# Kernel optimization log

Measured on AMD Instinct MI355X. Metric: run time of the kernel, lower is better.

The kernel has to match this reference:

```python
import jax, jax.numpy as jnp
import numpy as np
from jax import lax

N_QUBITS = 8
N_LAYERS = 7


def _conv(x, w, b, stride, pad):
    y = lax.conv_general_dilated(x, w, (stride, stride), [(pad, pad), (pad, pad)],
                                 dimension_numbers=('NCHW', 'OIHW', 'NCHW'))
    return y + b[None, :, None, None]


def _apply_1q(psi, M, q):
    # psi: (B, 2,2,...,2); apply 2x2 real matrix M on qubit q (axis q+1)
    a = q + 1
    pm = jnp.moveaxis(psi, a, 1)
    out = jnp.einsum('ij,bj...->bi...', M, pm)
    return jnp.moveaxis(out, 1, a)


def _apply_cnot(psi, c, t):
    ac, at = c + 1, t + 1
    pm = jnp.moveaxis(psi, (ac, at), (1, 2))
    top = pm[:, 0]
    bot = jnp.flip(pm[:, 1], axis=1)  # flip target when control=1
    pm = jnp.stack([top, bot], axis=1)
    return jnp.moveaxis(pm, (1, 2), (ac, at))


def _quantum(features, qw):
    psi = features / jnp.linalg.norm(features, axis=1, keepdims=True)
    B = psi.shape[0]
    psi = psi.reshape((B,) + (2,) * N_QUBITS)
    for l in range(N_LAYERS):
        for q in range(N_QUBITS):
            th = qw[l, q] / 2.0
            c, s = jnp.cos(th), jnp.sin(th)
            M = jnp.stack([jnp.stack([c, -s]), jnp.stack([s, c])])
            psi = _apply_1q(psi, M, q)
        for q in range(N_QUBITS - 1):
            psi = _apply_cnot(psi, q, q + 1)
    p = psi.reshape(B, 2, -1) ** 2
    return jnp.sum(p[:, 0], axis=1) - jnp.sum(p[:, 1], axis=1)  # <PauliZ(0)>


def setup_inputs() -> dict:
    key = jax.random.key(0)
    ks = jax.random.split(key, 20)
    def g(k, shape, fan_in):
        return jax.random.normal(k, shape, jnp.float32) * (1.0 / np.sqrt(fan_in))
    inp = {
        'x':  jax.random.normal(ks[0], (4096, 1, 64, 64), jnp.float32),
        'w1': g(ks[1], (4, 1, 5, 5), 25), 'b1': jnp.zeros((4,), jnp.float32),
        'w2': g(ks[2], (8, 4, 3, 3), 36), 'b2': jnp.zeros((8,), jnp.float32),
        'w3': g(ks[3], (16, 8, 3, 3), 72), 'b3': jnp.zeros((16,), jnp.float32),
        'wf': g(ks[4], (256, 64), 64), 'bf': jnp.zeros((256,), jnp.float32),
        'qw': jax.random.uniform(ks[5], (7, 8), jnp.float32, 0.0, 2 * np.pi),
        'wc1': g(ks[6], (200, 1), 1),   'bc1': jnp.zeros((200,), jnp.float32),
        'wc2': g(ks[7], (150, 200), 200), 'bc2': jnp.zeros((150,), jnp.float32),
        'wc3': g(ks[8], (100, 150), 150), 'bc3': jnp.zeros((100,), jnp.float32),
        'wc4': g(ks[9], (50, 100), 100),  'bc4': jnp.zeros((50,), jnp.float32),
        'wc5': g(ks[10], (1, 50), 50),    'bc5': jnp.zeros((1,), jnp.float32),
    }
    return inp


def reference(x, w1, b1, w2, b2, w3, b3, wf, bf, qw,
              wc1, bc1, wc2, bc2, wc3, bc3, wc4, bc4, wc5, bc5):
    # CNN feature extractor (dropout = identity at inference)
    h = jax.nn.relu(_conv(x, w1, b1, 2, 2))   # (B,4,32,32)
    h = jax.nn.relu(_conv(h, w2, b2, 2, 1))   # (B,8,16,16)
    h = jax.nn.relu(_conv(h, w3, b3, 1, 1))   # (B,16,16,16)
    B = h.shape[0]
    # AdaptiveAvgPool2d(2): 16x16 -> 2x2 via 8x8 non-overlapping means
    h = h.reshape(B, 16, 2, 8, 2, 8).mean(axis=(3, 5))  # (B,16,2,2)
    h = h.reshape(B, 64)
    feats = jax.nn.relu(h @ wf.T + bf)        # (B,256)
    # F.normalize(p=2, dim=1)
    feats = feats / jnp.maximum(jnp.linalg.norm(feats, axis=1, keepdims=True), 1e-12)
    # Batched 8-qubit statevector simulation (replaces per-sample Python loop)
    q = _quantum(feats, qw)[:, None]          # (B,1)
    # MLP classifier
    h = jax.nn.relu(q @ wc1.T + bc1)
    h = jax.nn.relu(h @ wc2.T + bc2)
    h = jax.nn.relu(h @ wc3.T + bc3)
    h = jax.nn.relu(h @ wc4.T + bc4)
    return jax.nn.sigmoid(h @ wc5.T + bc5)    # (B,1)
```

## Files before the change

kernel.cpp:

```cpp
#include <hip/hip_runtime.h>
#include <math.h>

typedef float v2f __attribute__((ext_vector_type(2)));
#define FMA2(a, b, c) __builtin_elementwise_fma((a), (b), (c))

__global__ __launch_bounds__(256, 8)
void convpool_kernel(const float* __restrict__ x,
                     const float* __restrict__ w1, const float* __restrict__ b1,
                     const float* __restrict__ w2, const float* __restrict__ b2,
                     const float* __restrict__ w3, const float* __restrict__ b3,
                     float* __restrict__ poolout)
{
    __shared__ __align__(16) float arena[4648];
    const int tid  = threadIdx.x;
    const int b    = blockIdx.x;
    const int lane = tid & 63;

    float wstage[7];
    #pragma unroll
    for (int j = 0; j < 7; j++) {
        const int s  = tid + 256 * j;
        const int oc = s / 100;
        const int r  = s - oc * 100;
        const int ic = r / 12;
        const int k  = r - ic * 12;
        wstage[j] = (s < 1600 && r < 96 && k < 9) ? w3[oc * 72 + ic * 9 + k] : 0.f;
    }
    const float bstage = (tid < 16) ? b3[tid] : 0.f;

    if (tid < 40) arena[4608 + tid] = 0.f;

    {
        const float* xb = x + (size_t)b * 4096;
        const int oh  = tid >> 3;
        const int ow  = tid & 7;
        const int ow0 = ow * 4;
        const int c0  = ow0 * 2 - 2;
        const bool cmL = (ow == 0);
        const bool cmR = (ow == 7);
        v2f aP[4][2];
        {
            const v2f b01 = {b1[0], b1[1]};
            const v2f b23 = {b1[2], b1[3]};
            #pragma unroll
            for (int p = 0; p < 4; p++) { aP[p][0] = b01; aP[p][1] = b23; }
        }
        #pragma unroll
        for (int kh = 0; kh < 5; kh++) {
            const int ih = oh * 2 - 2 + kh;
            if (ih >= 0 && ih < 64) {
                const float* row = xb + ih * 64;
                float colv[11];
                {
                    float v0 = row[cmL ? 0 : c0];
                    float v1 = row[cmL ? 0 : c0 + 1];
                    float vA = row[cmR ? 63 : c0 + 10];
                    colv[0]  = cmL ? 0.f : v0;
                    colv[1]  = cmL ? 0.f : v1;
                    colv[10] = cmR ? 0.f : vA;
                }
                {
                    const float4 m0 = *(const float4*)(row + c0 + 2);
                    const float4 m1 = *(const float4*)(row + c0 + 6);
                    colv[2] = m0.x; colv[3] = m0.y; colv[4] = m0.z; colv[5] = m0.w;
                    colv[6] = m1.x; colv[7] = m1.y; colv[8] = m1.z; colv[9] = m1.w;
                }
                #pragma unroll
                for (int kw = 0; kw < 5; kw++) {
                    const v2f w01 = {w1[kh * 5 + kw],      w1[25 + kh * 5 + kw]};
                    const v2f w23 = {w1[50 + kh * 5 + kw], w1[75 + kh * 5 + kw]};
                    #pragma unroll
                    for (int p = 0; p < 4; p++) {
                        const float c = colv[kw + 2 * p];
                        const v2f cs = {c, c};
                        aP[p][0] = FMA2(cs, w01, aP[p][0]);
                        aP[p][1] = FMA2(cs, w23, aP[p][1]);
                    }
                }
            }
        }
        const int bsw1 = (oh >> 1) & 1;
        float* obase = arena + oh * 36 + ((ow ^ bsw1) << 2);
        {
            float4 v;
            v.x = fmaxf(aP[0][0].x, 0.f); v.y = fmaxf(aP[1][0].x, 0.f);
            v.z = fmaxf(aP[2][0].x, 0.f); v.w = fmaxf(aP[3][0].x, 0.f);
            *(float4*)(obase) = v;
            v.x = fmaxf(aP[0][0].y, 0.f); v.y = fmaxf(aP[1][0].y, 0.f);
            v.z = fmaxf(aP[2][0].y, 0.f); v.w = fmaxf(aP[3][0].y, 0.f);
            *(float4*)(obase + 1152) = v;
            v.x = fmaxf(aP[0][1].x, 0.f); v.y = fmaxf(aP[1][1].x, 0.f);
            v.z = fmaxf(aP[2][1].x, 0.f); v.w = fmaxf(aP[3][1].x, 0.f);
            *(float4*)(obase + 2304) = v;
            v.x = fmaxf(aP[0][1].y, 0.f); v.y = fmaxf(aP[1][1].y, 0.f);
            v.z = fmaxf(aP[2][1].y, 0.f); v.w = fmaxf(aP[3][1].y, 0.f);
            *(float4*)(obase + 3456) = v;
        }
    }
    __syncthreads();

    v2f cacc[4];
    {
        const int oc0 = __builtin_amdgcn_readfirstlane(tid >> 6);
        const int oh  = lane >> 2;
        const int w   = lane & 3;
        {
            const v2f bb = {b2[oc0], b2[oc0 + 4]};
            #pragma unroll
            for (int p = 0; p < 4; p++) cacc[p] = bb;
        }
        #pragma unroll
        for (int ic = 0; ic < 4; ic++) {
            const float* base = arena + ic * 1152;
            const float* wA = w2 + ((oc0    ) * 4 + ic) * 9;
            const float* wB = w2 + ((oc0 + 4) * 4 + ic) * 9;
            #pragma unroll
            for (int kh = 0; kh < 3; kh++) {
                const int r2 = 2 * oh + kh - 1;
                const bool zr = (kh == 0) && (oh == 0);
                const int rc = zr ? 0 : r2;
                const int bsw = (rc >> 1) & 1;
                const float* row = zr ? (arena + 4608) : (base + rc * 36);
                const float4 qA = *(const float4*)(row + (((2 * w)     ^ bsw) << 2));
                const float4 qB = *(const float4*)(row + (((2 * w + 1) ^ bsw) << 2));
                const int sblk = (w == 0) ? bsw : ((2 * w - 1) ^ bsw);
                const float sv = row[(sblk << 2) + 3];
                float colv[9];
                colv[0] = (w == 0) ? 0.f : sv;
                colv[1] = qA.x; colv[2] = qA.y; colv[3] = qA.z; colv[4] = qA.w;
                colv[5] = qB.x; colv[6] = qB.y; colv[7] = qB.z; colv[8] = qB.w;
                #pragma unroll
                for (int kw = 0; kw < 3; kw++) {
                    const v2f wab = {wA[kh * 3 + kw], wB[kh * 3 + kw]};
                    #pragma unroll
                    for (int p = 0; p < 4; p++) {
                        const float c = colv[kw + 2 * p];
                        const v2f cs = {c, c};
                        cacc[p] = FMA2(cs, wab, cacc[p]);
                    }
                }
            }
        }
    }
    __syncthreads();

    for (int i = tid; i < 544; i += 256) {
        const int ch = i / 68, j = i - ch * 68;
        if (j < 18)      arena[ch * 360 + j] = 0.f;
        else if (j < 36) arena[ch * 360 + 17 * 20 + (j - 18)] = 0.f;
        else if (j < 52) arena[ch * 360 + (j - 35) * 20] = 0.f;
        else             arena[ch * 360 + (j - 51) * 20 + 17] = 0.f;
    }
    {
        const int oc0 = __builtin_amdgcn_readfirstlane(tid >> 6);
        const int oh  = lane >> 2, ow0 = (lane & 3) * 4;
        float* oA = arena + oc0 * 360       + (oh + 1) * 20 + ow0 + 1;
        float* oB = arena + (oc0 + 4) * 360 + (oh + 1) * 20 + ow0 + 1;
        oA[0] = fmaxf(cacc[0].x, 0.f); oA[1] = fmaxf(cacc[1].x, 0.f);
        oA[2] = fmaxf(cacc[2].x, 0.f); oA[3] = fmaxf(cacc[3].x, 0.f);
        oB[0] = fmaxf(cacc[0].y, 0.f); oB[1] = fmaxf(cacc[1].y, 0.f);
        oB[2] = fmaxf(cacc[2].y, 0.f); oB[3] = fmaxf(cacc[3].y, 0.f);
    }
    #pragma unroll
    for (int j = 0; j < 7; j++) {
        const int s = tid + 256 * j;
        if (s < 1600) arena[2880 + s] = wstage[j];
    }
    if (tid < 16) arena[4480 + tid] = bstage;
    __syncthreads();

    {
        const float* w3s = arena + 2880;
        const int oc = tid >> 4, s = tid & 15;
        const int tr = (s >> 2) * 4, tc = (s & 3) * 4;
        v2f acc2[4][2];
        const float bv = w3s[1600 + oc];
        #pragma unroll
        for (int r = 0; r < 4; r++) {
            acc2[r][0] = (v2f){bv, bv};
            acc2[r][1] = (v2f){bv, bv};
        }
        #pragma unroll
        for (int ic = 0; ic < 8; ic++) {
            const float* xc = arena + ic * 360;
            const float4 wv0 = *(const float4*)(w3s + oc * 100 + ic * 12);
            const float4 wv1 = *(const float4*)(w3s + oc * 100 + ic * 12 + 4);
            const float  wv8 = w3s[oc * 100 + ic * 12 + 8];
            const float wv[9] = {wv0.x, wv0.y, wv0.z, wv0.w, wv1.x, wv1.y, wv1.z, wv1.w, wv8};
            #pragma unroll
            for (int j = 0; j < 6; j++) {
                const float* rp = xc + (tr + j) * 20 + tc;
                const float4 qa = *(const float4*)(rp);
                const float4 qb = *(const float4*)(rp + 4);
                const v2f e0 = {qa.x, qa.y};
                const v2f o0 = {qa.y, qa.z};
                const v2f e1 = {qa.z, qa.w};
                const v2f o1 = {qa.w, qb.x};
                const v2f e2 = {qb.x, qb.y};
                #pragma unroll
                for (int r = 0; r < 4; r++) {
                    const int kh = j - r;
                    if (kh >= 0 && kh < 3) {
                        const v2f w0s = {wv[kh * 3 + 0], wv[kh * 3 + 0]};
                        const v2f w1s = {wv[kh * 3 + 1], wv[kh * 3 + 1]};
                        const v2f w2s = {wv[kh * 3 + 2], wv[kh * 3 + 2]};
                        acc2[r][0] = FMA2(e0, w0s, acc2[r][0]);
                        acc2[r][0] = FMA2(o0, w1s, acc2[r][0]);
                        acc2[r][0] = FMA2(e1, w2s, acc2[r][0]);
                        acc2[r][1] = FMA2(e1, w0s, acc2[r][1]);
                        acc2[r][1] = FMA2(o1, w1s, acc2[r][1]);
                        acc2[r][1] = FMA2(e2, w2s, acc2[r][1]);
                    }
                }
            }
        }
        float ps = 0.f;
        #pragma unroll
        for (int r = 0; r < 4; r++) {
            ps += fmaxf(acc2[r][0].x, 0.f);
            ps += fmaxf(acc2[r][0].y, 0.f);
            ps += fmaxf(acc2[r][1].x, 0.f);
            ps += fmaxf(acc2[r][1].y, 0.f);
        }
        ps += __shfl_xor(ps, 1, 64);
        ps += __shfl_xor(ps, 4, 64);
        if ((s & 5) == 0) {
            const int ii = s >> 3, jj = (s >> 1) & 1;
            poolout[b * 64 + oc * 4 + ii * 2 + jj] = ps * (1.f / 64.f);
        }
    }
}

__global__ __launch_bounds__(256)
void head_kernel(const float* __restrict__ poolin,
                 const float* __restrict__ wf, const float* __restrict__ bf,
                 const float* __restrict__ qw,
                 const float* __restrict__ wc1, const float* __restrict__ bc1,
                 const float* __restrict__ wc2, const float* __restrict__ bc2,
                 const float* __restrict__ wc3, const float* __restrict__ bc3,
                 const float* __restrict__ wc4, const float* __restrict__ bc4,
                 const float* __restrict__ wc5, const float* __restrict__ bc5,
                 float* __restrict__ out)
{
    __shared__ __align__(16) float pool_s[256];
    __shared__ __align__(16) float feats[1024];
    __shared__ __align__(16) float h1[800];
    __shared__ __align__(16) float h2[600];
    __shared__ __align__(16) float h3[400];
    __shared__ __align__(16) float h4[200];
    __shared__ float zbuf[4];
    __shared__ float csc[56], css[56];

    const int tid  = threadIdx.x;
    const int blk  = blockIdx.x;
    const int lane = tid & 63;
    const int wv   = tid >> 6;

    pool_s[tid] = poolin[(size_t)blk * 256 + tid];
    if (tid < 56) {
        float th = qw[tid] * 0.5f;
        csc[tid] = cosf(th);
        css[tid] = sinf(th);
    }
    __syncthreads();

    {
        float acc[4];
        const float bv = bf[tid];
        #pragma unroll
        for (int e = 0; e < 4; e++) acc[e] = bv;
        const float4* wr = (const float4*)(wf + tid * 64);
        #pragma unroll
        for (int kc = 0; kc < 4; kc++) {
            float4 w0 = wr[kc * 4 + 0], w1_ = wr[kc * 4 + 1], w2_ = wr[kc * 4 + 2], w3_ = wr[kc * 4 + 3];
            #pragma unroll
            for (int e = 0; e < 4; e++) {
                const float4* pp = (const float4*)(pool_s + e * 64 + kc * 16);
                float4 p0 = pp[0], p1 = pp[1], p2 = pp[2], p3 = pp[3];
                float a = acc[e];
                a = fmaf(w0.x, p0.x, a); a = fmaf(w0.y, p0.y, a); a = fmaf(w0.z, p0.z, a); a = fmaf(w0.w, p0.w, a);
                a = fmaf(w1_.x, p1.x, a); a = fmaf(w1_.y, p1.y, a); a = fmaf(w1_.z, p1.z, a); a = fmaf(w1_.w, p1.w, a);
                a = fmaf(w2_.x, p2.x, a); a = fmaf(w2_.y, p2.y, a); a = fmaf(w2_.z, p2.z, a); a = fmaf(w2_.w, p2.w, a);
                a = fmaf(w3_.x, p3.x, a); a = fmaf(w3_.y, p3.y, a); a = fmaf(w3_.z, p3.z, a); a = fmaf(w3_.w, p3.w, a);
                acc[e] = a;
            }
        }
        #pragma unroll
        for (int e = 0; e < 4; e++) feats[e * 256 + tid] = fmaxf(acc[e], 0.f);
    }
    __syncthreads();

    {
        const float* base = feats + wv * 256;
        float v0 = base[lane], v1 = base[64 + lane];
        float v2 = base[128 + lane], v3 = base[192 + lane];
        float ssq = v0 * v0 + v1 * v1 + v2 * v2 + v3 * v3;
        #pragma unroll
        for (int off = 1; off < 64; off <<= 1) ssq += __shfl_xor(ssq, off, 64);
        const float inv = 1.0f / fmaxf(sqrtf(ssq), 1e-12f);
        v0 *= inv; v1 *= inv; v2 *= inv; v3 *= inv;

        for (int l = 0; l < 7; l++) {
            {
                float c = csc[l * 8 + 0], s = css[l * 8 + 0];
                float n0 = c * v0 - s * v2, n2 = s * v0 + c * v2;
                float n1 = c * v1 - s * v3, n3 = s * v1 + c * v3;
                float c1 = csc[l * 8 + 1], s1 = css[l * 8 + 1];
                v0 = c1 * n0 - s1 * n1; v1 = s1 * n0 + c1 * n1;
                v2 = c1 * n2 - s1 * n3; v3 = s1 * n2 + c1 * n3;
            }
            #pragma unroll
            for (int q = 2; q < 8; q++) {
                const int m = 1 << (7 - q);
                const float c = csc[l * 8 + q], s = css[l * 8 + q];
                const float sgn = (lane & m) ? s : -s;
                float t0 = __shfl_xor(v0, m, 64);
                float t1 = __shfl_xor(v1, m, 64);
                float t2 = __shfl_xor(v2, m, 64);
                float t3 = __shfl_xor(v3, m, 64);
                v0 = fmaf(sgn, t0, c * v0);
                v1 = fmaf(sgn, t1, c * v1);
                v2 = fmaf(sgn, t2, c * v2);
                v3 = fmaf(sgn, t3, c * v3);
            }
            { float t = v2; v2 = v3; v3 = t; }
            v1 = __shfl_xor(v1, 32, 64);
            v3 = __shfl_xor(v3, 32, 64);
            #pragma unroll
            for (int q = 2; q < 7; q++) {
                const int mc = 1 << (7 - q), mt = 1 << (6 - q);
                float t0 = __shfl_xor(v0, mt, 64);
                float t1 = __shfl_xor(v1, mt, 64);
                float t2 = __shfl_xor(v2, mt, 64);
                float t3 = __shfl_xor(v3, mt, 64);
                if (lane & mc) { v0 = t0; v1 = t1; v2 = t2; v3 = t3; }
            }
        }
        float m0 = v0 * v0 + v1 * v1 - v2 * v2 - v3 * v3;
        #pragma unroll
        for (int off = 1; off < 64; off <<= 1) m0 += __shfl_xor(m0, off, 64);
        if (lane == 0) zbuf[wv] = m0;
    }
    __syncthreads();

    if (tid < 200) {
        const float w = wc1[tid], bv = bc1[tid];
        #pragma unroll
        for (int e = 0; e < 4; e++) h1[e * 200 + tid] = fmaxf(fmaf(zbuf[e], w, bv), 0.f);
    }
    __syncthreads();
    if (tid < 150) {
        float acc[4];
        const float bv = bc2[tid];
        #pragma unroll
        for (int e = 0; e < 4; e++) acc[e] = bv;
        const float4* wr = (const float4*)(wc2 + tid * 200);
        for (int kc = 0; kc < 25; kc++) {
            float4 wa = wr[2 * kc], wb = wr[2 * kc + 1];
            #pragma unroll
            for (int e = 0; e < 4; e++) {
                const float4* hp = (const float4*)(h1 + e * 200) + 2 * kc;
                float4 ha = hp[0], hb = hp[1];
                float a = acc[e];
                a = fmaf(wa.x, ha.x, a); a = fmaf(wa.y, ha.y, a); a = fmaf(wa.z, ha.z, a); a = fmaf(wa.w, ha.w, a);
                a = fmaf(wb.x, hb.x, a); a = fmaf(wb.y, hb.y, a); a = fmaf(wb.z, hb.z, a); a = fmaf(wb.w, hb.w, a);
                acc[e] = a;
            }
        }
        #pragma unroll
        for (int e = 0; e < 4; e++) h2[e * 150 + tid] = fmaxf(acc[e], 0.f);
    }
    __syncthreads();
    if (tid < 100) {
        float acc[4];
        const float bv = bc3[tid];
        #pragma unroll
        for (int e = 0; e < 4; e++) acc[e] = bv;
        const float2* wr = (const float2*)(wc3 + tid * 150);
        for (int k = 0; k < 75; k++) {
            float2 wa = wr[k];
            #pragma unroll
            for (int e = 0; e < 4; e++) {
                float2 hv = ((const float2*)(h2 + e * 150))[k];
                acc[e] = fmaf(wa.x, hv.x, fmaf(wa.y, hv.y, acc[e]));
            }
        }
        #pragma unroll
        for (int e = 0; e < 4; e++) h3[e * 100 + tid] = fmaxf(acc[e], 0.f);
    }
    __syncthreads();
    if (tid < 50) {
        float acc[4];
        const float bv = bc4[tid];
        #pragma unroll
        for (int e = 0; e < 4; e++) acc[e] = bv;
        const float4* wr = (const float4*)(wc4 + tid * 100);
        for (int kc = 0; kc < 25; kc++) {
            float4 wa = wr[kc];
            #pragma unroll
            for (int e = 0; e < 4; e++) {
                float4 hv = ((const float4*)(h3 + e * 100))[kc];
                float a = acc[e];
                a = fmaf(wa.x, hv.x, a); a = fmaf(wa.y, hv.y, a);
                a = fmaf(wa.z, hv.z, a); a = fmaf(wa.w, hv.w, a);
                acc[e] = a;
            }
        }
        #pragma unroll
        for (int e = 0; e < 4; e++) h4[e * 50 + tid] = fmaxf(acc[e], 0.f);
    }
    __syncthreads();
    if (tid < 4) {
        float acc = bc5[0];
        const float2* wr = (const float2*)wc5;
        #pragma unroll
        for (int k = 0; k < 25; k++) {
            float2 wa = wr[k];
            float2 hv = ((const float2*)(h4 + tid * 50))[k];
            acc = fmaf(wa.x, hv.x, fmaf(wa.y, hv.y, acc));
        }
        out[blk * 4 + tid] = 1.0f / (1.0f + expf(-acc));
    }
}

extern "C" void kernel_launch(void* const* d_in, const int* in_sizes, int n_in,
                              void* d_out, int out_size, void* d_ws, size_t ws_size,
                              hipStream_t stream) {
    const float* x   = (const float*)d_in[0];
    const float* w1  = (const float*)d_in[1];
    const float* b1  = (const float*)d_in[2];
    const float* w2  = (const float*)d_in[3];
    const float* b2  = (const float*)d_in[4];
    const float* w3  = (const float*)d_in[5];
    const float* b3  = (const float*)d_in[6];
    const float* wf  = (const float*)d_in[7];
    const float* bf  = (const float*)d_in[8];
    const float* qw  = (const float*)d_in[9];
    const float* wc1 = (const float*)d_in[10];
    const float* bc1 = (const float*)d_in[11];
    const float* wc2 = (const float*)d_in[12];
    const float* bc2 = (const float*)d_in[13];
    const float* wc3 = (const float*)d_in[14];
    const float* bc3 = (const float*)d_in[15];
    const float* wc4 = (const float*)d_in[16];
    const float* bc4 = (const float*)d_in[17];
    const float* wc5 = (const float*)d_in[18];
    const float* bc5 = (const float*)d_in[19];
    float* out = (float*)d_out;

    float* poolbuf = (float*)d_ws;

    convpool_kernel<<<4096, 256, 0, stream>>>(x, w1, b1, w2, b2, w3, b3, poolbuf);
    head_kernel<<<1024, 256, 0, stream>>>(poolbuf, wf, bf, qw,
                                          wc1, bc1, wc2, bc2, wc3, bc3,
                                          wc4, bc4, wc5, bc5, out);
}
```

Before: 212.3 us.

## Run MLP head per-wave per-sample with wave-local syncs instead of block barriers

```diff
diff --git a/kernel.cpp b/kernel.cpp
--- a/kernel.cpp
+++ b/kernel.cpp
@@ -3,6 +3,7 @@
 
 typedef float v2f __attribute__((ext_vector_type(2)));
 #define FMA2(a, b, c) __builtin_elementwise_fma((a), (b), (c))
+#define WAVE_SYNC() asm volatile("s_waitcnt lgkmcnt(0)" ::: "memory")
 
 __global__ __launch_bounds__(256, 8)
 void convpool_kernel(const float* __restrict__ x,
@@ -244,11 +245,7 @@
 {
     __shared__ __align__(16) float pool_s[256];
     __shared__ __align__(16) float feats[1024];
-    __shared__ __align__(16) float h1[800];
-    __shared__ __align__(16) float h2[600];
-    __shared__ __align__(16) float h3[400];
-    __shared__ __align__(16) float h4[200];
-    __shared__ float zbuf[4];
+    __shared__ __align__(16) float hbuf[4][512];
     __shared__ float csc[56], css[56];
 
     const int tid  = threadIdx.x;
@@ -290,6 +287,7 @@
     }
     __syncthreads();
 
+    float z;
     {
         const float* base = feats + wv * 256;
         float v0 = base[lane], v1 = base[64 + lane];
@@ -339,87 +337,81 @@
         float m0 = v0 * v0 + v1 * v1 - v2 * v2 - v3 * v3;
         #pragma unroll
         for (int off = 1; off < 64; off <<= 1) m0 += __shfl_xor(m0, off, 64);
-        if (lane == 0) zbuf[wv] = m0;
-    }
-    __syncthreads();
-
-    if (tid < 200) {
-        const float w = wc1[tid], bv = bc1[tid];
-        #pragma unroll
-        for (int e = 0; e < 4; e++) h1[e * 200 + tid] = fmaxf(fmaf(zbuf[e], w, bv), 0.f);
-    }
-    __syncthreads();
-    if (tid < 150) {
-        float acc[4];
-        const float bv = bc2[tid];
-        #pragma unroll
-        for (int e = 0; e < 4; e++) acc[e] = bv;
-        const float4* wr = (const float4*)(wc2 + tid * 200);
-        for (int kc = 0; kc < 25; kc++) {
-            float4 wa = wr[2 * kc], wb = wr[2 * kc + 1];
-            #pragma unroll
-            for (int e = 0; e < 4; e++) {
-                const float4* hp = (const float4*)(h1 + e * 200) + 2 * kc;
-                float4 ha = hp[0], hb = hp[1];
-                float a = acc[e];
+        z = m0;
+    }
+
+    float* H = hbuf[wv];
+
+    #pragma unroll
+    for (int t = 0; t < 4; t++) {
+        const int j = lane + 64 * t;
+        if (j < 200) H[j] = fmaxf(fmaf(z, wc1[j], bc1[j]), 0.f);
+    }
+    WAVE_SYNC();
+
+    #pragma unroll
+    for (int t = 0; t < 3; t++) {
+        const int j = lane + 64 * t;
+        if (j < 150) {
+            float a = bc2[j];
+            const float4* wr = (const float4*)(wc2 + j * 200);
+            const float4* hp = (const float4*)(H);
+            #pragma unroll 5
+            for (int kc = 0; kc < 25; kc++) {
+                const float4 wa = wr[2 * kc], wb = wr[2 * kc + 1];
+                const float4 ha = hp[2 * kc], hb = hp[2 * kc + 1];
                 a = fmaf(wa.x, ha.x, a); a = fmaf(wa.y, ha.y, a); a = fmaf(wa.z, ha.z, a); a = fmaf(wa.w, ha.w, a);
                 a = fmaf(wb.x, hb.x, a); a = fmaf(wb.y, hb.y, a); a = fmaf(wb.z, hb.z, a); a = fmaf(wb.w, hb.w, a);
-                acc[e] = a;
-            }
-        }
-        #pragma unroll
-        for (int e = 0; e < 4; e++) h2[e * 150 + tid] = fmaxf(acc[e], 0.f);
-    }
-    __syncthreads();
-    if (tid < 100) {
-        float acc[4];
-        const float bv = bc3[tid];
-        #pragma unroll
-        for (int e = 0; e < 4; e++) acc[e] = bv;
-        const float2* wr = (const float2*)(wc3 + tid * 150);
-        for (int k = 0; k < 75; k++) {
-            float2 wa = wr[k];
-            #pragma unroll
-            for (int e = 0; e < 4; e++) {
-                float2 hv = ((const float2*)(h2 + e * 150))[k];
-                acc[e] = fmaf(wa.x, hv.x, fmaf(wa.y, hv.y, acc[e]));
-            }
-        }
-        #pragma unroll
-        for (int e = 0; e < 4; e++) h3[e * 100 + tid] = fmaxf(acc[e], 0.f);
-    }
-    __syncthreads();
-    if (tid < 50) {
-        float acc[4];
-        const float bv = bc4[tid];
-        #pragma unroll
-        for (int e = 0; e < 4; e++) acc[e] = bv;
-        const float4* wr = (const float4*)(wc4 + tid * 100);
+            }
+            H[200 + j] = fmaxf(a, 0.f);
+        }
+    }
+    WAVE_SYNC();
+
+    #pragma unroll
+    for (int t = 0; t < 2; t++) {
+        const int j = lane + 64 * t;
+        if (j < 100) {
+            float a = bc3[j];
+            const float2* wr = (const float2*)(wc3 + j * 150);
+            const float2* hp = (const float2*)(H + 200);
+            #pragma unroll 5
+            for (int k = 0; k < 75; k++) {
+                const float2 wa = wr[k];
+                const float2 hv = hp[k];
+                a = fmaf(wa.x, hv.x, fmaf(wa.y, hv.y, a));
+            }
+            H[352 + j] = fmaxf(a, 0.f);
+        }
+    }
+    WAVE_SYNC();
+
+    if (lane < 50) {
+        float a = bc4[lane];
+        const float4* wr = (const float4*)(wc4 + lane * 100);
+        const float4* hp = (const float4*)(H + 352);
+        #pragma unroll 5
         for (int kc = 0; kc < 25; kc++) {
-            float4 wa = wr[kc];
-            #pragma unroll
-            for (int e = 0; e < 4; e++) {
-                float4 hv = ((const float4*)(h3 + e * 100))[kc];
-                float a = acc[e];
-                a = fmaf(wa.x, hv.x, a); a = fmaf(wa.y, hv.y, a);
-                a = fmaf(wa.z, hv.z, a); a = fmaf(wa.w, hv.w, a);
-                acc[e] = a;
-            }
-        }
-        #pragma unroll
-        for (int e = 0; e < 4; e++) h4[e * 50 + tid] = fmaxf(acc[e], 0.f);
-    }
-    __syncthreads();
-    if (tid < 4) {
-        float acc = bc5[0];
+            const float4 wa = wr[kc];
+            const float4 hv = hp[kc];
+            a = fmaf(wa.x, hv.x, a); a = fmaf(wa.y, hv.y, a);
+            a = fmaf(wa.z, hv.z, a); a = fmaf(wa.w, hv.w, a);
+        }
+        H[452 + lane] = fmaxf(a, 0.f);
+    }
+    WAVE_SYNC();
+
+    if (lane == 0) {
+        float a = bc5[0];
         const float2* wr = (const float2*)wc5;
+        const float2* hp = (const float2*)(H + 452);
         #pragma unroll
         for (int k = 0; k < 25; k++) {
-            float2 wa = wr[k];
-            float2 hv = ((const float2*)(h4 + tid * 50))[k];
-            acc = fmaf(wa.x, hv.x, fmaf(wa.y, hv.y, acc));
-        }
-        out[blk * 4 + tid] = 1.0f / (1.0f + expf(-acc));
+            const float2 wa = wr[k];
+            const float2 hv = hp[k];
+            a = fmaf(wa.x, hv.x, fmaf(wa.y, hv.y, a));
+        }
+        out[blk * 4 + wv] = 1.0f / (1.0f + expf(-a));
     }
 }
 
```

After: 239.5 us. +12.9%, slower.
